# Kernel optimization log

Measured on AMD Instinct MI355X. Metric: run time of the kernel, lower is better.

Reference implementation:

```python
import jax, jax.numpy as jnp
import numpy as np

SR = 22050
FMIN = 220.0
N_BINS = 84
BPO = 12
HOP = 512
NORM_P = 1
T_SAMPLES = 8388608  # 2**23 samples of audio


def _make_kernels():
    Q = 1.0 / (2.0 ** (1.0 / BPO) - 1.0)
    fftLen = 2 ** int(np.ceil(np.log2(np.ceil(Q * SR / FMIN))))  # 2048
    freqs = FMIN * 2.0 ** (np.arange(N_BINS) / float(BPO))
    temp = np.zeros((N_BINS, fftLen), dtype=np.complex64)
    for k in range(N_BINS):
        freq = freqs[k]
        l = np.ceil(Q * SR / freq)
        if l % 2 == 1:
            start = int(np.ceil(fftLen / 2.0 - l / 2.0)) - 1
        else:
            start = int(np.ceil(fftLen / 2.0 - l / 2.0))
        li = int(l)
        n = np.arange(li)
        hann = 0.5 - 0.5 * np.cos(2 * np.pi * n / li)  # periodic ('fftbins=True') hann
        idx = np.arange(np.floor(-l / 2.0), np.floor(l / 2.0))
        temp[k, start:start + li] = hann * np.exp(1j * 2 * np.pi * freq / SR * idx) / li
    spec = np.fft.fft(temp, axis=1)[:, : fftLen // 2 + 1]
    kr = spec.real.astype(np.float32)
    ki = spec.imag.astype(np.float32)
    # norm=1 branch: divide by L1 norm (over bins axis, dim=0) of complex magnitude
    mag = np.sqrt(kr ** 2 + ki ** 2)
    denom = np.sum(np.abs(mag), axis=0)  # shape [freq_bins]
    kr = (kr / denom).astype(np.float32)
    ki = (ki / denom).astype(np.float32)
    # Fourier kernels: freq_scale='no', windowing='no'
    freq_bins = fftLen // 2 + 1
    s = np.arange(fftLen, dtype=np.float64)
    kk = np.arange(freq_bins, dtype=np.float64)
    ang = 2 * np.pi * np.outer(kk, s) / fftLen  # [freq_bins, fftLen]
    wsin = np.sin(ang).astype(np.float32)
    wcos = np.cos(ang).astype(np.float32)
    return kr, ki, wcos, wsin


def setup_inputs() -> dict:
    key = jax.random.key(0)
    x = jax.random.normal(key, (T_SAMPLES,), dtype=jnp.float32)
    kr, ki, wcos, wsin = _make_kernels()
    return {
        "x": x,
        "wcos": jnp.asarray(wcos),
        "wsin": jnp.asarray(wsin),
        "kr": jnp.asarray(kr),
        "ki": jnp.asarray(ki),
    }


def reference(x, wcos, wsin, kr, ki):
    fftLen = wcos.shape[1]  # 2048
    n_frames = (x.shape[0] - fftLen) // HOP + 1  # static under jit
    # frame the signal: equivalent to conv1d(x, w, stride=HOP) with kernels w
    idx = jnp.arange(n_frames)[:, None] * HOP + jnp.arange(fftLen)[None, :]
    frames = x[idx]  # [n_frames, fftLen]
    fourier_real = jnp.einsum("fn,kn->kf", frames, wcos)  # [freq_bins, n_frames]
    fourier_imag = jnp.einsum("fn,kn->kf", frames, wsin)
    cqt_real = kr @ fourier_real - ki @ fourier_imag  # [n_bins, n_frames]
    cqt_imag = kr @ fourier_imag + ki @ fourier_real
    cqt = jnp.sqrt(cqt_real ** 2 + cqt_imag ** 2)
    return cqt[None]  # [1, n_bins, n_frames]
```

## Files before the change

kernel.cpp:

```cpp
#include <hip/hip_runtime.h>


#define HOPS 512
#define NBINS 84
#define FREQB 1025
#define NFRAMES 16381
#define TSAMP 8388608
#define SPAN 34304
#define KP16 138

typedef short bf16x8 __attribute__((ext_vector_type(8)));
typedef float f32x16 __attribute__((ext_vector_type(16)));

union B8 { struct { ushort4 lo, hi; } p; bf16x8 v; uint4 u; };

__device__ __forceinline__ unsigned short f32_to_bf16(float f) {
    union { float f; unsigned u; } v; v.f = f;
    return (unsigned short)((v.u + 0x7FFFu + ((v.u >> 16) & 1u)) >> 16);
}
__device__ __forceinline__ unsigned pk_bf16(float lo, float hi) {
    return (unsigned)f32_to_bf16(lo) | ((unsigned)f32_to_bf16(hi) << 16);
}
__device__ __forceinline__ bf16x8 pack8(const float* s) {
    B8 r;
    r.u.x = pk_bf16(s[0], s[1]); r.u.y = pk_bf16(s[2], s[3]);
    r.u.z = pk_bf16(s[4], s[5]); r.u.w = pk_bf16(s[6], s[7]);
    return r.v;
}

__device__ __forceinline__ float cos_rev(float r) { return __builtin_amdgcn_cosf(r); }
__device__ __forceinline__ float sin_rev(float r) { return __builtin_amdgcn_sinf(r); }

__global__ __launch_bounds__(64) void aprep_kernel(
    const float* __restrict__ kr, const float* __restrict__ ki,
    unsigned short* __restrict__ Apf)
{
    const int bid = blockIdx.x;
    const int mt = bid / KP16, k16 = bid % KP16;
    const int l = threadIdx.x;
    const int c32 = l & 31, h = l >> 5;
    const int row = mt * 32 + c32;
    const int b = row >> 1, im = row & 1;
    const bool bok = b < NBINS;
    const float* cosp = (im ? ki : kr) + (size_t)(bok ? b : 0) * FREQB;
    const float* sinp = (im ? kr : ki) + (size_t)(bok ? b : 0) * FREQB;
    const float ssign = im ? 1.f : -1.f;

    unsigned short o[8];
    #pragma unroll
    for (int j = 0; j < 8; ++j) {
        int k = k16 * 16 + h * 8 + j;
        float v = 0.f;
        if (bok) {
            if (k <= 1024)       v = cosp[k];
            else if (k <= 2049)  v = ssign * sinp[k - 1025];
        }
        o[j] = f32_to_bf16(v);
    }
    uint4 pk;
    pk.x = (unsigned)o[0] | ((unsigned)o[1] << 16);
    pk.y = (unsigned)o[2] | ((unsigned)o[3] << 16);
    pk.z = (unsigned)o[4] | ((unsigned)o[5] << 16);
    pk.w = (unsigned)o[6] | ((unsigned)o[7] << 16);
    *(uint4*)(Apf + (size_t)bid * 512 + (size_t)l * 8) = pk;
}

__global__ __launch_bounds__(256) void wfused_kernel(
    const unsigned short* __restrict__ Apf, unsigned short* __restrict__ Wpf)
{
    __shared__ float4 red[3][4][64];

    const int bid = blockIdx.x;
    const int mt = bid >> 6, nt = bid & 63;
    const int t = threadIdx.x;
    const int w = t >> 6, l = t & 63;
    const int c32 = l & 31, h = l >> 5;
    const int n = nt * 32 + c32;

    f32x16 acc;
    #pragma unroll
    for (int i = 0; i < 16; ++i) acc[i] = 0.f;

    const int k0 = w * 33;
    const int kcnt = (w < 3) ? 33 : 30;
    const unsigned short* ap = Apf + (size_t)(mt * KP16 + k0) * 512 + (size_t)l * 8;

    for (int i = 0; i < kcnt; ++i) {
        const int k16 = k0 + i;
        B8 bf; bf.u = *(const uint4*)(ap + (size_t)i * 512);
        float tv[8];
        const int kb = k16 * 16 + h * 8;
        if (k16 <= 63) {
            #pragma unroll
            for (int j = 0; j < 8; ++j) {
                int p = __mul24(kb + j, n) & 2047;
                tv[j] = cos_rev((float)p * (1.f / 2048.f));
            }
        } else if (k16 >= 65 && k16 <= 127) {
            #pragma unroll
            for (int j = 0; j < 8; ++j) {
                int p = __mul24(kb + j - 1025, n) & 2047;
                tv[j] = sin_rev((float)p * (1.f / 2048.f));
            }
        } else {
            #pragma unroll
            for (int j = 0; j < 8; ++j) {
                int k = kb + j;
                float v = 0.f;
                if (k <= 1024) {
                    int p = __mul24(k, n) & 2047;
                    v = cos_rev((float)p * (1.f / 2048.f));
                } else if (k <= 2049) {
                    int p = __mul24(k - 1025, n) & 2047;
                    v = sin_rev((float)p * (1.f / 2048.f));
                }
                tv[j] = v;
            }
        }
        acc = __builtin_amdgcn_mfma_f32_32x32x16_bf16(pack8(tv), bf.v, acc, 0, 0, 0);
    }

    if (w > 0) {
        #pragma unroll
        for (int q = 0; q < 4; ++q)
            red[w - 1][q][l] = make_float4(acc[4*q+0], acc[4*q+1], acc[4*q+2], acc[4*q+3]);
    }
    __syncthreads();
    if (w == 0) {
        #pragma unroll
        for (int s = 0; s < 3; ++s) {
            #pragma unroll
            for (int q = 0; q < 4; ++q) {
                float4 v = red[s][q][l];
                acc[4*q+0] += v.x; acc[4*q+1] += v.y;
                acc[4*q+2] += v.z; acc[4*q+3] += v.w;
            }
        }
        #pragma unroll
        for (int g = 0; g < 4; ++g) {
            uint2 qo;
            qo.x = pk_bf16(acc[4*g+0], acc[4*g+1]);
            qo.y = pk_bf16(acc[4*g+2], acc[4*g+3]);
            size_t off = (size_t)(mt * 128 + nt * 2 + (g >> 1)) * 512
                       + (size_t)(c32 + 32 * (g & 1)) * 8 + 4 * h;
            *(uint2*)(Wpf + off) = qo;
        }
    }
}

__global__ __launch_bounds__(768) void cqt_kernel(
    const float* __restrict__ x, const unsigned short* __restrict__ Wpf,
    float* __restrict__ out)
{
    __shared__ __align__(16) unsigned short xl[SPAN];

    const int t = threadIdx.x;
    const int f0 = blockIdx.x * 64;
    const long S0 = (long)f0 * HOPS;
    const int valid = (int)((TSAMP - S0) < (long)SPAN ? (TSAMP - S0) : (long)SPAN);

    #pragma unroll
    for (int i = 0; i < 12; ++i) {
        int idx4 = t + i * 768;
        if (idx4 < 8576) {
            int s = idx4 * 4;
            float4 v = make_float4(0.f, 0.f, 0.f, 0.f);
            if (s + 4 <= valid) v = *(const float4*)(x + S0 + s);
            ushort4 o;
            o.x = f32_to_bf16(v.x); o.y = f32_to_bf16(v.y);
            o.z = f32_to_bf16(v.z); o.w = f32_to_bf16(v.w);
            int byte = idx4 * 8;
            int bsw = byte ^ (((byte >> 10) & 7) << 4);
            *(ushort4*)((char*)xl + bsw) = o;
        }
    }
    __syncthreads();

    const int w = t >> 6, l = t & 63;
    const int mg = w >> 1, fg = w & 1;
    const int c32 = l & 31, h = l >> 5;

    const unsigned short* apf = Wpf + (size_t)mg * (128 * 512) + (size_t)l * 8;
    const int byteBase = (fg * 32 + c32) * 1024 + h * 16;

    f32x16 acc;
    #pragma unroll
    for (int i = 0; i < 16; ++i) acc[i] = 0.f;

    auto ldsB = [&](int k16) -> bf16x8 {
        int byte = byteBase + k16 * 32;
        int bsw = byte ^ (((byte >> 10) & 7) << 4);
        B8 r;
        r.u = *(const uint4*)((const char*)xl + bsw);
        return r.v;
    };

    uint4 Abuf[2][8];
    #pragma unroll
    for (int j = 0; j < 8; ++j)
        Abuf[0][j] = *(const uint4*)(apf + (size_t)j * 512);

    #pragma unroll
    for (int c = 0; c < 16; ++c) {
        const int cur = c & 1, nxt = cur ^ 1;
        if (c < 15) {
            #pragma unroll
            for (int j = 0; j < 8; ++j)
                Abuf[nxt][j] = *(const uint4*)(apf + (size_t)((c + 1) * 8 + j) * 512);
        }
        #pragma unroll
        for (int j = 0; j < 8; ++j) {
            B8 af; af.u = Abuf[cur][j];
            acc = __builtin_amdgcn_mfma_f32_32x32x16_bf16(af.v, ldsB(c * 8 + j), acc, 0, 0, 0);
        }
    }

    const int f = f0 + fg * 32 + c32;
    if (f < NFRAMES) {
        #pragma unroll
        for (int rp = 0; rp < 4; ++rp) {
            int base = mg * 32 + 8 * rp + 4 * h;
            int b0 = base >> 1;
            float r0 = acc[4 * rp + 0], i0 = acc[4 * rp + 1];
            float r1 = acc[4 * rp + 2], i1 = acc[4 * rp + 3];
            if (b0 < NBINS)
                out[(size_t)b0 * NFRAMES + f] = sqrtf(r0 * r0 + i0 * i0);
            if (b0 + 1 < NBINS)
                out[(size_t)(b0 + 1) * NFRAMES + f] = sqrtf(r1 * r1 + i1 * i1);
        }
    }
}

extern "C" void kernel_launch(void* const* d_in, const int* in_sizes, int n_in,
                              void* d_out, int out_size, void* d_ws, size_t ws_size,
                              hipStream_t stream) {
    const float* x    = (const float*)d_in[0];
    const float* kr   = (const float*)d_in[3];
    const float* ki   = (const float*)d_in[4];
    float* out = (float*)d_out;

    unsigned short* Wpf = (unsigned short*)d_ws;
    unsigned short* Apf = (unsigned short*)((char*)d_ws + 786432);

    aprep_kernel<<<dim3(6 * KP16), dim3(64), 0, stream>>>(kr, ki, Apf);
    wfused_kernel<<<dim3(384), dim3(256), 0, stream>>>(Apf, Wpf);
    cqt_kernel<<<dim3(256), dim3(768), 0, stream>>>(x, Wpf, out);
}
```

Baseline: 120.9 us.

## Fuse A-matrix prep into the W-build kernel via shared-memory staging

Removes the separate aprep kernel. Each W-build block now converts its 32-row slice of kr/ki to bf16 in LDS and reuses it for two N-tiles, using 8 waves per block. This saves one kernel launch and the global write/read of the packed A matrix. In exchange, the A slice is rebuilt redundantly in every block, and the roughly 156KB of LDS limits each CU to one block, with only 192 blocks across the CUs.

```diff
diff --git a/kernel.cpp b/kernel.cpp
--- a/kernel.cpp
+++ b/kernel.cpp
@@ -7,7 +7,6 @@
 #define NFRAMES 16381
 #define TSAMP 8388608
 #define SPAN 34304
-#define KP16 138
 
 typedef short bf16x8 __attribute__((ext_vector_type(8)));
 typedef float f32x16 __attribute__((ext_vector_type(16)));
@@ -31,63 +30,63 @@
 __device__ __forceinline__ float cos_rev(float r) { return __builtin_amdgcn_cosf(r); }
 __device__ __forceinline__ float sin_rev(float r) { return __builtin_amdgcn_sinf(r); }
 
-__global__ __launch_bounds__(64) void aprep_kernel(
+__global__ __launch_bounds__(512) void wfused2_kernel(
     const float* __restrict__ kr, const float* __restrict__ ki,
-    unsigned short* __restrict__ Apf)
+    unsigned short* __restrict__ Wpf)
 {
+    __shared__ __align__(16) unsigned short As[129 * 512];
+    __shared__ float4 red[2][3][4][64];
+
     const int bid = blockIdx.x;
-    const int mt = bid / KP16, k16 = bid % KP16;
-    const int l = threadIdx.x;
+    const int mt = bid >> 5, ntg = bid & 31;
+    const int t = threadIdx.x;
+
+    for (int item = t; item < 32 * 258; item += 512) {
+        const int row = item / 258, o = item % 258;
+        const int arow = mt * 32 + row;
+        const int b = arow >> 1, im = arow & 1;
+        const bool bok = b < NBINS;
+        const float* cosp = (im ? ki : kr) + (size_t)(bok ? b : 0) * FREQB;
+        const float* sinp = (im ? kr : ki) + (size_t)(bok ? b : 0) * FREQB;
+        const float ssign = im ? 1.f : -1.f;
+        const int k0 = o * 8;
+        unsigned short ov[8];
+        #pragma unroll
+        for (int j = 0; j < 8; ++j) {
+            int k = k0 + j;
+            float v = 0.f;
+            if (bok) {
+                if (k <= 1024)       v = cosp[k];
+                else if (k <= 2049)  v = ssign * sinp[k - 1025];
+            }
+            ov[j] = f32_to_bf16(v);
+        }
+        uint4 pk;
+        pk.x = (unsigned)ov[0] | ((unsigned)ov[1] << 16);
+        pk.y = (unsigned)ov[2] | ((unsigned)ov[3] << 16);
+        pk.z = (unsigned)ov[4] | ((unsigned)ov[5] << 16);
+        pk.w = (unsigned)ov[6] | ((unsigned)ov[7] << 16);
+        const int k16 = o >> 1, h = o & 1;
+        *(uint4*)(As + (size_t)k16 * 512 + (size_t)(h * 32 + row) * 8) = pk;
+    }
+    __syncthreads();
+
+    const int w = t >> 6, l = t & 63;
+    const int nl = w >> 2, s = w & 3;
     const int c32 = l & 31, h = l >> 5;
-    const int row = mt * 32 + c32;
-    const int b = row >> 1, im = row & 1;
-    const bool bok = b < NBINS;
-    const float* cosp = (im ? ki : kr) + (size_t)(bok ? b : 0) * FREQB;
-    const float* sinp = (im ? kr : ki) + (size_t)(bok ? b : 0) * FREQB;
-    const float ssign = im ? 1.f : -1.f;
-
-    unsigned short o[8];
-    #pragma unroll
-    for (int j = 0; j < 8; ++j) {
-        int k = k16 * 16 + h * 8 + j;
-        float v = 0.f;
-        if (bok) {
-            if (k <= 1024)       v = cosp[k];
-            else if (k <= 2049)  v = ssign * sinp[k - 1025];
-        }
-        o[j] = f32_to_bf16(v);
-    }
-    uint4 pk;
-    pk.x = (unsigned)o[0] | ((unsigned)o[1] << 16);
-    pk.y = (unsigned)o[2] | ((unsigned)o[3] << 16);
-    pk.z = (unsigned)o[4] | ((unsigned)o[5] << 16);
-    pk.w = (unsigned)o[6] | ((unsigned)o[7] << 16);
-    *(uint4*)(Apf + (size_t)bid * 512 + (size_t)l * 8) = pk;
-}
-
-__global__ __launch_bounds__(256) void wfused_kernel(
-    const unsigned short* __restrict__ Apf, unsigned short* __restrict__ Wpf)
-{
-    __shared__ float4 red[3][4][64];
-
-    const int bid = blockIdx.x;
-    const int mt = bid >> 6, nt = bid & 63;
-    const int t = threadIdx.x;
-    const int w = t >> 6, l = t & 63;
-    const int c32 = l & 31, h = l >> 5;
+    const int nt = ntg * 2 + nl;
     const int n = nt * 32 + c32;
 
     f32x16 acc;
     #pragma unroll
     for (int i = 0; i < 16; ++i) acc[i] = 0.f;
 
-    const int k0 = w * 33;
-    const int kcnt = (w < 3) ? 33 : 30;
-    const unsigned short* ap = Apf + (size_t)(mt * KP16 + k0) * 512 + (size_t)l * 8;
+    const int k0 = s * 33;
+    const int kcnt = (s < 3) ? 33 : 30;
 
     for (int i = 0; i < kcnt; ++i) {
         const int k16 = k0 + i;
-        B8 bf; bf.u = *(const uint4*)(ap + (size_t)i * 512);
+        B8 bf; bf.u = *(const uint4*)(As + (size_t)k16 * 512 + (size_t)l * 8);
         float tv[8];
         const int kb = k16 * 16 + h * 8;
         if (k16 <= 63) {
@@ -120,18 +119,19 @@
         acc = __builtin_amdgcn_mfma_f32_32x32x16_bf16(pack8(tv), bf.v, acc, 0, 0, 0);
     }
 
-    if (w > 0) {
+    if (s > 0) {
         #pragma unroll
         for (int q = 0; q < 4; ++q)
-            red[w - 1][q][l] = make_float4(acc[4*q+0], acc[4*q+1], acc[4*q+2], acc[4*q+3]);
+            red[nl][s - 1][q][l] = make_float4(acc[4*q+0], acc[4*q+1],
+                                               acc[4*q+2], acc[4*q+3]);
     }
     __syncthreads();
-    if (w == 0) {
-        #pragma unroll
-        for (int s = 0; s < 3; ++s) {
+    if (s == 0) {
+        #pragma unroll
+        for (int e = 0; e < 3; ++e) {
             #pragma unroll
             for (int q = 0; q < 4; ++q) {
-                float4 v = red[s][q][l];
+                float4 v = red[nl][e][q][l];
                 acc[4*q+0] += v.x; acc[4*q+1] += v.y;
                 acc[4*q+2] += v.z; acc[4*q+3] += v.w;
             }
@@ -240,9 +240,7 @@
     float* out = (float*)d_out;
 
     unsigned short* Wpf = (unsigned short*)d_ws;
-    unsigned short* Apf = (unsigned short*)((char*)d_ws + 786432);
-
-    aprep_kernel<<<dim3(6 * KP16), dim3(64), 0, stream>>>(kr, ki, Apf);
-    wfused_kernel<<<dim3(384), dim3(256), 0, stream>>>(Apf, Wpf);
+
+    wfused2_kernel<<<dim3(192), dim3(512), 0, stream>>>(kr, ki, Wpf);
     cqt_kernel<<<dim3(256), dim3(768), 0, stream>>>(x, Wpf, out);
 }
```

After: 152.8 us. 1.26x slower.
